# Kernel optimization log

Measured on AMD Instinct MI355X. Metric: run time of the kernel, lower is better.

The kernel has to match this reference:

```python
import math
import jax, jax.numpy as jnp
import numpy as np

# Neuron / simulation constants (from docstring defaults)
THETA = 10.0
TAU_SR = 10.0
TAU_REF = 1.0
SCALE_REF = 2.0
SCALE_RHO = 1.0
TS = 1.0
T_SAMPLE = 300


def _alpha_kernel(tau, mult, eps_tol):
    # Faithful to slayer._calculateAlphaKernel: eps(t) = mult * t/tau * exp(1 - t/tau),
    # truncated once |eps| < eps_tol and t > tau.
    vals = []
    for t in np.arange(0.0, T_SAMPLE, TS):
        v = mult * t / tau * math.exp(1.0 - t / tau)
        if abs(v) < eps_tol and t > tau:
            break
        vals.append(v)
    return np.asarray(vals, np.float32)


def psp(spike, srm_kernel):
    # slayerCuda.conv: causal temporal convolution psp[t] = sum_k f[k] * spike[t-k]
    N, C, H, W, T = spike.shape
    x = spike.reshape(-1, 1, T)                       # (B,1,T), B = N*C*H*W
    K = srm_kernel.shape[0]
    w = jnp.flip(srm_kernel).reshape(1, 1, K).astype(x.dtype)
    y = jax.lax.conv_general_dilated(
        x, w, window_strides=(1,), padding=[(K - 1, 0)],
        dimension_numbers=('NCH', 'OIH', 'NCH'))
    return y.reshape(N, C, H, W, T)


def get_spikes(u2, ref_kernel):
    # slayerCuda.getSpikes: sequential scan over time. At each step the effective
    # membrane potential is u[t] plus pending refractory contributions from past
    # spikes; a spike (value 1/Ts) fires when u_eff >= theta and injects the
    # refractory kernel into future timesteps.
    # u2: (B, T); ref_kernel: (K,) with ref_kernel[0] == 0 (alpha kernel).
    B, T = u2.shape
    K = ref_kernel.shape[0]
    ref_tail = ref_kernel[1:].astype(u2.dtype)        # contributions to t+1..t+K-1

    def step(pend, u_t):
        u_eff = u_t + pend[:, 0]
        s = (u_eff >= THETA).astype(u2.dtype)
        pend = jnp.concatenate([pend[:, 1:], jnp.zeros_like(pend[:, :1])], axis=1)
        pend = pend + s[:, None] * ref_tail[None, :]
        return pend, (s / TS, u_eff)

    pend0 = jnp.zeros((B, K - 1), u2.dtype)
    _, (s, u_mod) = jax.lax.scan(step, pend0, u2.T)
    return s.T, u_mod.T


def setup_inputs() -> dict:
    key = jax.random.key(0)
    k1, = jax.random.split(key, 1)
    N, C, H, W, T = 4, 16, 32, 32, T_SAMPLE
    u = jax.random.uniform(k1, (N, C, H, W, T), dtype=jnp.float32)
    spike_in = (u < 0.05).astype(jnp.float32) / TS
    srm_kernel = jnp.asarray(_alpha_kernel(TAU_SR, 1.0, 0.01))
    ref_kernel = jnp.asarray(_alpha_kernel(TAU_REF, -SCALE_REF * THETA, 0.01))
    return {"spike_in": spike_in, "srm_kernel": srm_kernel, "ref_kernel": ref_kernel}


def reference(spike_in, srm_kernel, ref_kernel):
    # psp (exponential alpha PSP conv) followed by spike generation scan
    u = psp(spike_in, srm_kernel)                     # (N,C,H,W,T)
    T = u.shape[-1]
    s, _ = get_spikes(u.reshape(-1, T), ref_kernel)
    return s.reshape(spike_in.shape)
```

## Files before the change

kernel.cpp:

```cpp
#include <hip/hip_runtime.h>
#include <hip/hip_bf16.h>


#define T_LEN 300
#define CH 20
#define NCHUNK 15
#define KS 77
#define KR 10
#define THETA_V 10.0f

__global__ __launch_bounds__(256)
__attribute__((amdgpu_waves_per_eu(1, 1)))
void spike_layer_kernel(
    const float* __restrict__ spike_in,
    const float* __restrict__ srm, int srm_len,
    const float* __restrict__ refk, int ref_len,
    float* __restrict__ out, int B)
{
    int b = blockIdx.x * blockDim.x + threadIdx.x;
    if (b >= B) return;

    const float* row  = spike_in + (size_t)b * T_LEN;
    float*       orow = out      + (size_t)b * T_LEN;

    float srm_r[KS];
#pragma unroll
    for (int i = 0; i < KS; ++i) srm_r[i] = (i < srm_len) ? srm[i] : 0.0f;

    float rt[KR];
#pragma unroll
    for (int i = 0; i < KR; ++i) rt[i] = (i + 1 < ref_len) ? refk[i + 1] : 0.0f;

    float hist[KS + CH];
#pragma unroll
    for (int i = 0; i < KS; ++i) hist[i] = 0.0f;

    float pend[KR];
#pragma unroll
    for (int i = 0; i < KR; ++i) pend[i] = 0.0f;

    float nxt[CH];
    {
        const float4* p = (const float4*)row;
#pragma unroll
        for (int i = 0; i < CH / 4; ++i) {
            float4 v = p[i];
            nxt[4*i+0] = v.x; nxt[4*i+1] = v.y; nxt[4*i+2] = v.z; nxt[4*i+3] = v.w;
        }
    }

#pragma unroll 1
    for (int ch = 0; ch < NCHUNK; ++ch) {
#pragma unroll
        for (int i = 0; i < CH; ++i) hist[KS + i] = nxt[i];

        if (ch + 1 < NCHUNK) {
            const float4* p = (const float4*)(row + (ch + 1) * CH);
#pragma unroll
            for (int i = 0; i < CH / 4; ++i) {
                float4 v = p[i];
                nxt[4*i+0] = v.x; nxt[4*i+1] = v.y; nxt[4*i+2] = v.z; nxt[4*i+3] = v.w;
            }
        }

        float u[CH];
#pragma unroll
        for (int c = 0; c < CH; ++c) u[c] = 0.0f;
#pragma unroll
        for (int j = 0; j < KS; ++j) {
            float w = srm_r[j];
#pragma unroll
            for (int c = 0; c < CH; ++c)
                u[c] = fmaf(w, hist[KS + c - j], u[c]);
        }

#pragma unroll
        for (int c = 0; c < CH; ++c) {
            float u_eff = u[c] + pend[0];
            float s = (u_eff >= THETA_V) ? 1.0f : 0.0f;
#pragma unroll
            for (int i = 0; i < KR - 1; ++i) pend[i] = fmaf(s, rt[i], pend[i + 1]);
            pend[KR - 1] = s * rt[KR - 1];
            u[c] = s;
        }

        {
            float4* op = (float4*)(orow + ch * CH);
#pragma unroll
            for (int i = 0; i < CH / 4; ++i) {
                float4 v;
                v.x = u[4*i+0]; v.y = u[4*i+1]; v.z = u[4*i+2]; v.w = u[4*i+3];
                op[i] = v;
            }
        }

#pragma unroll
        for (int i = 0; i < KS; ++i) hist[i] = hist[i + CH];
    }
}

extern "C" void kernel_launch(void* const* d_in, const int* in_sizes, int n_in,
                              void* d_out, int out_size, void* d_ws, size_t ws_size,
                              hipStream_t stream) {
    const float* spike_in = (const float*)d_in[0];
    const float* srm      = (const float*)d_in[1];
    const float* refk     = (const float*)d_in[2];
    float* out = (float*)d_out;

    int srm_len = in_sizes[1];
    int ref_len = in_sizes[2];
    int B = in_sizes[0] / T_LEN;

    int block = 256;
    int grid = (B + block - 1) / block;
    spike_layer_kernel<<<grid, block, 0, stream>>>(spike_in, srm, srm_len,
                                                   refk, ref_len, out, B);
}
```

Before: 181.3 us.

## Move convolution history window from registers to shared memory

Stores the 77-sample input history for each thread in LDS, strided by thread so accesses avoid bank conflicts, instead of holding it in a register array. The convolution loop is reorganised to stream each history value once and apply it to every affected output. This frees roughly a hundred VGPRs per thread. The cost is an LDS read per history value and an LDS copy to shift the window each chunk, about 97 KB of shared memory per block. The shared array is sized WIN=97 although only 77 slots are used.

```diff
diff --git a/kernel.cpp b/kernel.cpp
--- a/kernel.cpp
+++ b/kernel.cpp
@@ -8,8 +8,10 @@
 #define KS 77
 #define KR 10
 #define THETA_V 10.0f
+#define NTH 256
+#define WIN 97
 
-__global__ __launch_bounds__(256)
+__global__ __launch_bounds__(NTH)
 __attribute__((amdgpu_waves_per_eu(1, 1)))
 void spike_layer_kernel(
     const float* __restrict__ spike_in,
@@ -17,7 +19,10 @@
     const float* __restrict__ refk, int ref_len,
     float* __restrict__ out, int B)
 {
-    int b = blockIdx.x * blockDim.x + threadIdx.x;
+    __shared__ float hist[WIN * NTH];
+
+    const int tid = threadIdx.x;
+    int b = blockIdx.x * NTH + tid;
     if (b >= B) return;
 
     const float* row  = spike_in + (size_t)b * T_LEN;
@@ -31,9 +36,8 @@
 #pragma unroll
     for (int i = 0; i < KR; ++i) rt[i] = (i + 1 < ref_len) ? refk[i + 1] : 0.0f;
 
-    float hist[KS + CH];
 #pragma unroll
-    for (int i = 0; i < KS; ++i) hist[i] = 0.0f;
+    for (int i = 0; i < WIN; ++i) hist[i * NTH + tid] = 0.0f;
 
     float pend[KR];
 #pragma unroll
@@ -51,8 +55,27 @@
 
 #pragma unroll 1
     for (int ch = 0; ch < NCHUNK; ++ch) {
+        float u[CH];
 #pragma unroll
-        for (int i = 0; i < CH; ++i) hist[KS + i] = nxt[i];
+        for (int c = 0; c < CH; ++c) u[c] = 0.0f;
+
+#pragma unroll
+        for (int i = 1; i < WIN + CH; ++i) {
+            if (i >= WIN && i - KS >= CH) break;
+            float h = (i < KS) ? hist[i * NTH + tid] : nxt[i - KS];
+            const int clo = (i - KS < 0) ? 0 : i - KS;
+            const int chi = (i - 1 < CH - 1) ? i - 1 : CH - 1;
+#pragma unroll
+            for (int c = clo; c <= chi; ++c)
+                u[c] = fmaf(srm_r[c + KS - i], h, u[c]);
+        }
+
+#pragma unroll
+        for (int i = 1; i < KS - CH; ++i)
+            hist[i * NTH + tid] = hist[(i + CH) * NTH + tid];
+#pragma unroll
+        for (int i = KS - CH; i < KS; ++i)
+            hist[i * NTH + tid] = nxt[i - (KS - CH)];
 
         if (ch + 1 < NCHUNK) {
             const float4* p = (const float4*)(row + (ch + 1) * CH);
@@ -61,17 +84,6 @@
                 float4 v = p[i];
                 nxt[4*i+0] = v.x; nxt[4*i+1] = v.y; nxt[4*i+2] = v.z; nxt[4*i+3] = v.w;
             }
-        }
-
-        float u[CH];
-#pragma unroll
-        for (int c = 0; c < CH; ++c) u[c] = 0.0f;
-#pragma unroll
-        for (int j = 0; j < KS; ++j) {
-            float w = srm_r[j];
-#pragma unroll
-            for (int c = 0; c < CH; ++c)
-                u[c] = fmaf(w, hist[KS + c - j], u[c]);
         }
 
 #pragma unroll
@@ -93,9 +105,6 @@
                 op[i] = v;
             }
         }
-
-#pragma unroll
-        for (int i = 0; i < KS; ++i) hist[i] = hist[i + CH];
     }
 }
 
@@ -111,7 +120,7 @@
     int ref_len = in_sizes[2];
     int B = in_sizes[0] / T_LEN;
 
-    int block = 256;
+    int block = NTH;
     int grid = (B + block - 1) / block;
     spike_layer_kernel<<<grid, block, 0, stream>>>(spike_in, srm, srm_len,
                                                    refk, ref_len, out, B);
```

Result: no change. 180.4 us (-0.5%).

## Split each row's PSP convolution across four threads using an LDS spike history

Applied to the files above, without the earlier changes.

Each block now handles 64 rows with 256 threads. Four threads per row each compute 8 of the 32 timesteps per chunk of the PSP convolution, reading spike history from a padded shared-memory buffer instead of per-thread register arrays. The sequential spike-generation scan stays on one thread per row (q==0) and reads the membrane potentials back from LDS. This gives four times as many threads for the FMA-heavy convolution and cuts register pressure. In exchange it adds LDS traffic, three barriers per chunk, and leaves three quarters of the threads idle during the scan. The grid assumes B is divisible by 64, with no bounds check.

```diff
diff --git a/kernel.cpp b/kernel.cpp
--- a/kernel.cpp
+++ b/kernel.cpp
@@ -3,99 +3,183 @@
 
 
 #define T_LEN 300
-#define CH 20
-#define NCHUNK 15
+#define NB 64
+#define NTH 256
+#define TC 32
+#define NFULL 9
+#define TAIL 12
 #define KS 77
 #define KR 10
 #define THETA_V 10.0f
-
-__global__ __launch_bounds__(256)
-__attribute__((amdgpu_waves_per_eu(1, 1)))
-void spike_layer_kernel(
+#define STR 65
+#define U_COLS 32
+#define SP_OFF (U_COLS * STR)
+#define SP_COLS 108
+#define LDS_FLOATS (SP_OFF + SP_COLS * STR)
+
+__global__ __launch_bounds__(NTH, 4) void spike_layer_kernel(
     const float* __restrict__ spike_in,
     const float* __restrict__ srm, int srm_len,
     const float* __restrict__ refk, int ref_len,
-    float* __restrict__ out, int B)
+    float* __restrict__ out)
 {
-    int b = blockIdx.x * blockDim.x + threadIdx.x;
-    if (b >= B) return;
-
-    const float* row  = spike_in + (size_t)b * T_LEN;
-    float*       orow = out      + (size_t)b * T_LEN;
+    __shared__ float lds[LDS_FLOATS];
+
+    const int tid = threadIdx.x;
+    const int n   = tid & 63;
+    const int q   = tid >> 6;
+    const int row = blockIdx.x * NB + n;
+
+    const float* inR  = spike_in + (size_t)row * T_LEN;
+    float*       outR = out      + (size_t)row * T_LEN;
 
     float srm_r[KS];
 #pragma unroll
     for (int i = 0; i < KS; ++i) srm_r[i] = (i < srm_len) ? srm[i] : 0.0f;
 
-    float rt[KR];
-#pragma unroll
-    for (int i = 0; i < KR; ++i) rt[i] = (i + 1 < ref_len) ? refk[i + 1] : 0.0f;
-
-    float hist[KS + CH];
-#pragma unroll
-    for (int i = 0; i < KS; ++i) hist[i] = 0.0f;
-
-    float pend[KR];
-#pragma unroll
-    for (int i = 0; i < KR; ++i) pend[i] = 0.0f;
-
-    float nxt[CH];
+    float rt[KR], pend[KR];
+#pragma unroll
+    for (int i = 0; i < KR; ++i) {
+        rt[i]   = (i + 1 < ref_len) ? refk[i + 1] : 0.0f;
+        pend[i] = 0.0f;
+    }
+
+    float* uB   = &lds[n];
+    float* spB  = &lds[SP_OFF + n];
+    float* spQ8 = spB + (q * 8) * STR;
+    float* uQ8  = uB  + (q * 8) * STR;
+    float* chB  = spB + q * STR;
+
+    float4 g0 = *(const float4*)(inR + q * 8);
+    float4 g1 = *(const float4*)(inR + q * 8 + 4);
+#pragma unroll
+    for (int k = 0; k < 8; ++k) {
+        chB[(4 * k) * STR]      = 0.0f;
+        chB[(4 * k + 32) * STR] = 0.0f;
+        if (k < 3) chB[(4 * k + 64) * STR] = 0.0f;
+    }
     {
-        const float4* p = (const float4*)row;
-#pragma unroll
-        for (int i = 0; i < CH / 4; ++i) {
-            float4 v = p[i];
-            nxt[4*i+0] = v.x; nxt[4*i+1] = v.y; nxt[4*i+2] = v.z; nxt[4*i+3] = v.w;
-        }
-    }
+        float* d = spB + (76 + q * 8) * STR;
+        d[0] = g0.x; d[STR] = g0.y; d[2*STR] = g0.z; d[3*STR] = g0.w;
+        d[4*STR] = g1.x; d[5*STR] = g1.y; d[6*STR] = g1.z; d[7*STR] = g1.w;
+    }
+    __syncthreads();
 
 #pragma unroll 1
-    for (int ch = 0; ch < NCHUNK; ++ch) {
-#pragma unroll
-        for (int i = 0; i < CH; ++i) hist[KS + i] = nxt[i];
-
-        if (ch + 1 < NCHUNK) {
-            const float4* p = (const float4*)(row + (ch + 1) * CH);
-#pragma unroll
-            for (int i = 0; i < CH / 4; ++i) {
-                float4 v = p[i];
-                nxt[4*i+0] = v.x; nxt[4*i+1] = v.y; nxt[4*i+2] = v.z; nxt[4*i+3] = v.w;
-            }
-        }
-
-        float u[CH];
-#pragma unroll
-        for (int c = 0; c < CH; ++c) u[c] = 0.0f;
-#pragma unroll
-        for (int j = 0; j < KS; ++j) {
-            float w = srm_r[j];
-#pragma unroll
-            for (int c = 0; c < CH; ++c)
-                u[c] = fmaf(w, hist[KS + c - j], u[c]);
-        }
-
-#pragma unroll
-        for (int c = 0; c < CH; ++c) {
-            float u_eff = u[c] + pend[0];
-            float s = (u_eff >= THETA_V) ? 1.0f : 0.0f;
+    for (int ch = 0; ch < NFULL; ++ch) {
+        if (ch < NFULL - 1) {
+            const float* p = inR + (ch + 1) * TC + q * 8;
+            g0 = *(const float4*)p;
+            g1 = *(const float4*)(p + 4);
+        } else {
+            if (q == 0)      { g0 = *(const float4*)(inR + 288); g1 = *(const float4*)(inR + 292); }
+            else if (q == 1) { g0 = *(const float4*)(inR + 296); }
+        }
+
+        float u[8];
+#pragma unroll
+        for (int k = 0; k < 8; ++k) u[k] = 0.0f;
+#pragma unroll
+        for (int R = 83; R >= 0; --R) {
+            float h = spQ8[R * STR];
+#pragma unroll
+            for (int k = 0; k < 8; ++k) {
+                const int j = k + 76 - R;
+                if (j >= 0 && j <= 76) u[k] = fmaf(srm_r[j], h, u[k]);
+            }
+        }
+#pragma unroll
+        for (int k = 0; k < 8; ++k) uQ8[k * STR] = u[k];
+
+        __syncthreads();
+
+        if (q == 0) {
+#pragma unroll
+            for (int c = 0; c < U_COLS; ++c) {
+                float ue = uB[c * STR] + pend[0];
+                float s  = (ue >= THETA_V) ? 1.0f : 0.0f;
+#pragma unroll
+                for (int i = 0; i < KR - 1; ++i) pend[i] = fmaf(s, rt[i], pend[i + 1]);
+                pend[KR - 1] = s * rt[KR - 1];
+                uB[c * STR] = s;
+            }
+        }
+
+#pragma unroll
+        for (int k = 0; k < 8; ++k) {
+            float* cp = chB + (4 * k) * STR;
+            float a = cp[32 * STR];
+            float b = cp[64 * STR];
+            if (k < 3) {
+                float c2 = cp[96 * STR];
+                cp[0] = a; cp[32 * STR] = b; cp[64 * STR] = c2;
+            } else {
+                cp[0] = a; cp[32 * STR] = b;
+            }
+        }
+
+        __syncthreads();
+
+        if (ch < NFULL - 1) {
+            float* d = spB + (76 + q * 8) * STR;
+            d[0] = g0.x; d[STR] = g0.y; d[2*STR] = g0.z; d[3*STR] = g0.w;
+            d[4*STR] = g1.x; d[5*STR] = g1.y; d[6*STR] = g1.z; d[7*STR] = g1.w;
+        } else {
+            if (q == 0) {
+                float* d = spB + 76 * STR;
+                d[0] = g0.x; d[STR] = g0.y; d[2*STR] = g0.z; d[3*STR] = g0.w;
+                d[4*STR] = g1.x; d[5*STR] = g1.y; d[6*STR] = g1.z; d[7*STR] = g1.w;
+            } else if (q == 1) {
+                float* d = spB + 84 * STR;
+                d[0] = g0.x; d[STR] = g0.y; d[2*STR] = g0.z; d[3*STR] = g0.w;
+            }
+        }
+
+        {
+            float* o = outR + ch * TC + q * 8;
+            float4 s0, s1;
+            s0.x = uQ8[0];       s0.y = uQ8[STR];     s0.z = uQ8[2*STR]; s0.w = uQ8[3*STR];
+            s1.x = uQ8[4*STR];   s1.y = uQ8[5*STR];   s1.z = uQ8[6*STR]; s1.w = uQ8[7*STR];
+            *(float4*)o = s0;
+            *(float4*)(o + 4) = s1;
+        }
+
+        __syncthreads();
+    }
+
+    {
+        float* spQ3 = spB + (q * 3) * STR;
+        float u[3] = {0.0f, 0.0f, 0.0f};
+#pragma unroll
+        for (int R = 78; R >= 0; --R) {
+            float h = spQ3[R * STR];
+#pragma unroll
+            for (int k = 0; k < 3; ++k) {
+                const int j = k + 76 - R;
+                if (j >= 0 && j <= 76) u[k] = fmaf(srm_r[j], h, u[k]);
+            }
+        }
+        float* uQ3 = uB + (q * 3) * STR;
+#pragma unroll
+        for (int k = 0; k < 3; ++k) uQ3[k * STR] = u[k];
+    }
+    __syncthreads();
+    if (q == 0) {
+#pragma unroll
+        for (int c = 0; c < TAIL; ++c) {
+            float ue = uB[c * STR] + pend[0];
+            float s  = (ue >= THETA_V) ? 1.0f : 0.0f;
 #pragma unroll
             for (int i = 0; i < KR - 1; ++i) pend[i] = fmaf(s, rt[i], pend[i + 1]);
             pend[KR - 1] = s * rt[KR - 1];
-            u[c] = s;
-        }
-
-        {
-            float4* op = (float4*)(orow + ch * CH);
-#pragma unroll
-            for (int i = 0; i < CH / 4; ++i) {
-                float4 v;
-                v.x = u[4*i+0]; v.y = u[4*i+1]; v.z = u[4*i+2]; v.w = u[4*i+3];
-                op[i] = v;
-            }
-        }
-
-#pragma unroll
-        for (int i = 0; i < KS; ++i) hist[i] = hist[i + CH];
+            uB[c * STR] = s;
+        }
+    }
+    __syncthreads();
+    {
+        float* uQ3 = uB + (q * 3) * STR;
+        float* o   = outR + 288 + q * 3;
+        o[0] = uQ3[0]; o[1] = uQ3[STR]; o[2] = uQ3[2 * STR];
     }
 }
 
@@ -111,8 +195,7 @@
     int ref_len = in_sizes[2];
     int B = in_sizes[0] / T_LEN;
 
-    int block = 256;
-    int grid = (B + block - 1) / block;
-    spike_layer_kernel<<<grid, block, 0, stream>>>(spike_in, srm, srm_len,
-                                                   refk, ref_len, out, B);
+    int grid = B / NB;
+    spike_layer_kernel<<<grid, NTH, 0, stream>>>(spike_in, srm, srm_len,
+                                                 refk, ref_len, out);
 }
```

After: 185.0 us. 1.02x slower.
